# Optimization experiments

Measured on AMD Instinct MI355X. Metric: run time of the kernel, lower is better.

The kernel has to match this reference:

```python
import jax, jax.numpy as jnp
import numpy as np

B, C, H, W = 4, 256, 64, 64
N = H * W


def _conv1x1(x, w, b):
    # x: [B,C,H,W], w: [O,C], b: [O]  (1x1 conv == per-pixel linear)
    return jnp.einsum('bchw,oc->bohw', x, w) + b[None, :, None, None]


def setup_inputs() -> dict:
    key = jax.random.key(0)
    ks = jax.random.split(key, 11)
    s = 1.0 / np.sqrt(C)
    x = jax.random.normal(ks[0], (B, C, H, W), dtype=jnp.float32)
    mkw = lambda k: jax.random.normal(k, (C, C), dtype=jnp.float32) * s
    mkb = lambda k: jax.random.normal(k, (C,), dtype=jnp.float32) * 0.01
    return {
        'x': x,
        'w_teta': mkw(ks[1]), 'b_teta': mkb(ks[2]),
        'w_fi': mkw(ks[3]), 'b_fi': mkb(ks[4]),
        'w_gi': mkw(ks[5]), 'b_gi': mkb(ks[6]),
        'w_o1': mkw(ks[7]), 'b_o1': mkb(ks[8]),
        'w_o2': mkw(ks[9]), 'b_o2': mkb(ks[10]),
    }


def reference(x, w_teta, b_teta, w_fi, b_fi, w_gi, b_gi, w_o1, b_o1, w_o2, b_o2):
    b, c, h, w = x.shape
    n = h * w
    # 1x1 projections, flattened to [B,C,N]
    x1 = _conv1x1(x, w_teta, b_teta).reshape(b, c, n)
    x2 = _conv1x1(x, w_fi, b_fi).reshape(b, c, n)
    x3 = _conv1x1(x, w_gi, b_gi).reshape(b, c, n)
    # NOTE: original uses .view (memory reinterpretation), NOT transpose
    x1 = x1.reshape(b, n, c)
    x3 = x3.reshape(b, n, c)
    scores = jnp.einsum('bnc,bcm->bnm', x1, x2)      # [B,N,N]
    s_row = jax.nn.softmax(scores, axis=2)
    s_col = jax.nn.softmax(scores, axis=1)
    y1 = jnp.einsum('bnm,bmc->bnc', s_row, x3)       # [B,N,C]
    y2 = jnp.einsum('bnm,bmc->bnc', s_col, x3)
    # transpose(1,2) then view -> contiguous transpose + reshape
    y1 = jnp.swapaxes(y1, 1, 2).reshape(b, c, h, w)
    y2 = jnp.swapaxes(y2, 1, 2).reshape(b, c, h, w)
    o1 = _conv1x1(y1, w_o1, b_o1)
    o2 = _conv1x1(y2, w_o2, b_o2)
    xx = jnp.concatenate([x, x], axis=1)             # [B,2C,H,W]
    agg = jnp.concatenate([o1, o2], axis=1)
    return jax.nn.relu(xx + agg)
```

## Files before the change

### kernel.cpp

```cpp
#include <hip/hip_runtime.h>

#define BB   4
#define CC   256
#define NPIX 4096
#define AST2 40
#define YST  72

typedef __attribute__((ext_vector_type(8)))  short bf16x8;
typedef __attribute__((ext_vector_type(8)))  _Float16 f16x8;
typedef __attribute__((ext_vector_type(4)))  short short4v;
typedef __attribute__((ext_vector_type(16))) float f32x16;

__device__ __forceinline__ short f2h(float f) {
    _Float16 h = (_Float16)f;
    return __builtin_bit_cast(short, h);
}
__device__ __forceinline__ int cdrow(int r, int l5) {
    return (r & 3) + 8 * (r >> 2) + 4 * l5;
}
__device__ __forceinline__ short s_enc(float v) {
    float c = fmaxf(fminf(v, 127.9f), -127.9f);
    return (short)__float2int_rn(c * 256.0f);
}
__device__ __forceinline__ float s_dec(short v) {
    return (float)v * (1.0f / 256.0f);
}

__device__ __forceinline__ void mfma_core_f16(
    const short* __restrict__ A, const short* __restrict__ B, f32x16 acc[2][2])
{
    __shared__ short LA[128 * AST2], LB[128 * AST2];
    const int t = threadIdx.x;
    const int lane = t & 63, w = t >> 6;
    const int l31 = lane & 31, l5 = lane >> 5;
    const int nq = (w & 1) * 64, mq = (w >> 1) * 64;
    const int sr = t >> 1;
    const int sk = (t & 1) * 16;
    const size_t gs = (size_t)sr * 256 + sk;
    const int ls = sr * AST2 + sk;

    bf16x8 rA0 = *(const bf16x8*)(A + gs);
    bf16x8 rA1 = *(const bf16x8*)(A + gs + 8);
    bf16x8 rB0 = *(const bf16x8*)(B + gs);
    bf16x8 rB1 = *(const bf16x8*)(B + gs + 8);

    for (int k0 = 0; k0 < 256; k0 += 32) {
        __syncthreads();
        *(bf16x8*)&LA[ls]     = rA0;
        *(bf16x8*)&LA[ls + 8] = rA1;
        *(bf16x8*)&LB[ls]     = rB0;
        *(bf16x8*)&LB[ls + 8] = rB1;
        __syncthreads();
        if (k0 + 32 < 256) {
            size_t g = gs + k0 + 32;
            rA0 = *(const bf16x8*)(A + g);
            rA1 = *(const bf16x8*)(A + g + 8);
            rB0 = *(const bf16x8*)(B + g);
            rB1 = *(const bf16x8*)(B + g + 8);
        }
#pragma unroll
        for (int ks = 0; ks < 2; ks++) {
            f16x8 a[2], b[2];
#pragma unroll
            for (int s = 0; s < 2; s++) {
                a[s] = *(const f16x8*)&LA[(nq + s * 32 + l31) * AST2 + ks * 16 + l5 * 8];
                b[s] = *(const f16x8*)&LB[(mq + s * 32 + l31) * AST2 + ks * 16 + l5 * 8];
            }
#pragma unroll
            for (int s = 0; s < 2; s++)
#pragma unroll
                for (int u = 0; u < 2; u++)
                    acc[s][u] = __builtin_amdgcn_mfma_f32_32x32x16_f16(a[s], b[u], acc[s][u], 0, 0, 0);
        }
    }
}


__global__ __launch_bounds__(256) void pack_w5(
    const float* __restrict__ w0, const float* __restrict__ w1,
    const float* __restrict__ w2, const float* __restrict__ w3,
    const float* __restrict__ w4, short* __restrict__ wall)
{
    int which = blockIdx.y;
    const float* w = which == 0 ? w0 : which == 1 ? w1 : which == 2 ? w2
                   : which == 3 ? w3 : w4;
    int idx = blockIdx.x * 1024 + threadIdx.x * 4;
    float4 v = *(const float4*)(w + idx);
    short4v h;
    h.x = f2h(v.x); h.y = f2h(v.y); h.z = f2h(v.z); h.w = f2h(v.w);
    *(short4v*)(wall + which * 65536 + idx) = h;
}

__global__ __launch_bounds__(256) void pack_t_f16(
    const float* __restrict__ in, short* __restrict__ o16)
{
    __shared__ short T[32][36];
    const int b  = blockIdx.z;
    const int n0 = blockIdx.x * 32;
    const int c0 = blockIdx.y * 32;
    const float* src = in + (size_t)b * CC * NPIX;
    const int t = threadIdx.x;
    const int r = t >> 3, q = t & 7;
    float4 v = *(const float4*)(src + (size_t)(c0 + r) * NPIX + n0 + q * 4);
    T[q * 4 + 0][r] = f2h(v.x);
    T[q * 4 + 1][r] = f2h(v.y);
    T[q * 4 + 2][r] = f2h(v.z);
    T[q * 4 + 3][r] = f2h(v.w);
    __syncthreads();
    short4v o;
    o.x = T[r][q * 4 + 0];
    o.y = T[r][q * 4 + 1];
    o.z = T[r][q * 4 + 2];
    o.w = T[r][q * 4 + 3];
    size_t oo = (size_t)b * CC * NPIX + (size_t)(n0 + r) * 256 + c0 + q * 4;
    *(short4v*)(o16 + oo) = o;
}

__global__ __launch_bounds__(256) void tr16_cn(
    const short* __restrict__ in, short* __restrict__ outp)
{
    __shared__ short T[32][33];
    const int b  = blockIdx.z;
    const int n0 = blockIdx.x * 32;
    const int c0 = blockIdx.y * 32;
    const short* src = in + (size_t)b * CC * NPIX;
    short* dst = outp + (size_t)b * CC * NPIX;
    const int t = threadIdx.x;
    const int r = t >> 3, q = t & 7;
    short4v v = *(const short4v*)(src + (size_t)(c0 + r) * NPIX + n0 + q * 4);
    T[q * 4 + 0][r] = v.x;
    T[q * 4 + 1][r] = v.y;
    T[q * 4 + 2][r] = v.z;
    T[q * 4 + 3][r] = v.w;
    __syncthreads();
    short4v o;
    o.x = T[r][q * 4 + 0];
    o.y = T[r][q * 4 + 1];
    o.z = T[r][q * 4 + 2];
    o.w = T[r][q * 4 + 3];
    *(short4v*)(dst + (size_t)(n0 + r) * 256 + c0 + q * 4) = o;
}

__global__ __launch_bounds__(256) void packVt_bf(
    const short* __restrict__ x3f, short* __restrict__ Vt)
{
    __shared__ short T[32][33];
    const int b  = blockIdx.z;
    const int m0 = blockIdx.x * 32;
    const int c0 = blockIdx.y * 32;
    const short* in = x3f + (size_t)b * CC * NPIX;
    short* out = Vt + (size_t)b * CC * NPIX;
    const int t = threadIdx.x;
    const int r = t >> 3, q = t & 7;
    short4v v = *(const short4v*)(in + (size_t)(m0 + r) * CC + c0 + q * 4);
    T[q * 4 + 0][r] = v.x;
    T[q * 4 + 1][r] = v.y;
    T[q * 4 + 2][r] = v.z;
    T[q * 4 + 3][r] = v.w;
    __syncthreads();
    short4v o;
    o.x = T[r][q * 4 + 0];
    o.y = T[r][q * 4 + 1];
    o.z = T[r][q * 4 + 2];
    o.w = T[r][q * 4 + 3];
    *(short4v*)(out + (size_t)(c0 + r) * NPIX + m0 + q * 4) = o;
}


__global__ __launch_bounds__(256) void proj_mfma(
    const short* __restrict__ wpf, const short* __restrict__ xtf,
    const float* __restrict__ b_teta, const float* __restrict__ b_fi,
    const float* __restrict__ b_gi,
    short* __restrict__ x1f, short* __restrict__ x2f, short* __restrict__ x3f)
{
    const int z = blockIdx.z, p = z >> 2, b = z & 3;
    const int n0 = blockIdx.x * 128, c0 = blockIdx.y * 128;
    const size_t CN = (size_t)CC * NPIX;
    const short* Ah = wpf + p * 65536 + c0 * 256;
    const short* Bh = xtf + (size_t)b * CN + (size_t)n0 * 256;
    const float* bias = p == 0 ? b_teta : p == 1 ? b_fi : b_gi;
    short* dst = p == 0 ? x1f : p == 1 ? x2f : x3f;

    f32x16 acc[2][2] = {};
    mfma_core_f16(Ah, Bh, acc);

    const int t = threadIdx.x, lane = t & 63, w = t >> 6;
    const int l31 = lane & 31, l5 = lane >> 5;
    const int aq = (w & 1) * 64, bq = (w >> 1) * 64;
#pragma unroll
    for (int s = 0; s < 2; s++)
#pragma unroll
        for (int u = 0; u < 2; u++)
#pragma unroll
            for (int r = 0; r < 16; r++) {
                int c = c0 + aq + s * 32 + cdrow(r, l5);
                int n = n0 + bq + u * 32 + l31;
                float v = acc[s][u][r] + bias[c];
                size_t o = (size_t)b * CN + (size_t)c * NPIX + n;
                dst[o] = f2h(v);
            }
}

__global__ __launch_bounds__(256, 2) void scores_mfma(
    const short* __restrict__ x1f, const short* __restrict__ x2tf,
    short* __restrict__ S16, float* __restrict__ pm, float* __restrict__ pl)
{
    __shared__ short LA[256 * AST2];
    __shared__ short LB[128 * AST2];
    const int m0 = blockIdx.x * 128, n0 = blockIdx.y * 256;
    const short* A = x1f + (size_t)n0 * 256;
    const short* B = x2tf + (size_t)m0 * 256;

    const int t = threadIdx.x, lane = t & 63, w = t >> 6;
    const int l31 = lane & 31, l5 = lane >> 5;
    const int h = w & 1, g = w >> 1;

    const size_t gsA = (size_t)t * 256;
    const int lsA = t * AST2;
    const int srB = t >> 1, skB = (t & 1) * 16;
    const size_t gsB = (size_t)srB * 256 + skB;
    const int lsB = srB * AST2 + skB;

    bf16x8 rA0 = *(const bf16x8*)(A + gsA);
    bf16x8 rA1 = *(const bf16x8*)(A + gsA + 8);
    bf16x8 rA2 = *(const bf16x8*)(A + gsA + 16);
    bf16x8 rA3 = *(const bf16x8*)(A + gsA + 24);
    bf16x8 rB0 = *(const bf16x8*)(B + gsB);
    bf16x8 rB1 = *(const bf16x8*)(B + gsB + 8);

    f32x16 acc[4][2] = {};

    for (int k0 = 0; k0 < 256; k0 += 32) {
        __syncthreads();
        *(bf16x8*)&LA[lsA]      = rA0;
        *(bf16x8*)&LA[lsA + 8]  = rA1;
        *(bf16x8*)&LA[lsA + 16] = rA2;
        *(bf16x8*)&LA[lsA + 24] = rA3;
        *(bf16x8*)&LB[lsB]      = rB0;
        *(bf16x8*)&LB[lsB + 8]  = rB1;
        __syncthreads();
        if (k0 + 32 < 256) {
            size_t gA = gsA + k0 + 32;
            size_t gB = gsB + k0 + 32;
            rA0 = *(const bf16x8*)(A + gA);
            rA1 = *(const bf16x8*)(A + gA + 8);
            rA2 = *(const bf16x8*)(A + gA + 16);
            rA3 = *(const bf16x8*)(A + gA + 24);
            rB0 = *(const bf16x8*)(B + gB);
            rB1 = *(const bf16x8*)(B + gB + 8);
        }
#pragma unroll
        for (int ks = 0; ks < 2; ks++) {
            f16x8 a[4], b[2];
#pragma unroll
            for (int s = 0; s < 4; s++)
                a[s] = *(const f16x8*)&LA[(h * 128 + s * 32 + l31) * AST2 + ks * 16 + l5 * 8];
#pragma unroll
            for (int u = 0; u < 2; u++)
                b[u] = *(const f16x8*)&LB[(g * 64 + u * 32 + l31) * AST2 + ks * 16 + l5 * 8];
#pragma unroll
            for (int s = 0; s < 4; s++)
#pragma unroll
                for (int u = 0; u < 2; u++)
                    acc[s][u] = __builtin_amdgcn_mfma_f32_32x32x16_f16(a[s], b[u], acc[s][u], 0, 0, 0);
        }
    }

#pragma unroll
    for (int s = 0; s < 4; s++)
#pragma unroll
        for (int u = 0; u < 2; u++)
#pragma unroll
            for (int r = 0; r < 16; r++) {
                int n = n0 + h * 128 + s * 32 + cdrow(r, l5);
                int m = m0 + g * 64 + u * 32 + l31;
                S16[(size_t)n * NPIX + m] = s_enc(acc[s][u][r]);
            }

#pragma unroll
    for (int u = 0; u < 2; u++) {
        float vmax = -1e30f;
#pragma unroll
        for (int s = 0; s < 4; s++)
#pragma unroll
            for (int r = 0; r < 16; r++) vmax = fmaxf(vmax, acc[s][u][r]);
        float vsum = 0.0f;
#pragma unroll
        for (int s = 0; s < 4; s++)
#pragma unroll
            for (int r = 0; r < 16; r++) vsum += __expf(acc[s][u][r] - vmax);
        float vmax2 = __shfl_xor(vmax, 32, 64);
        float vsum2 = __shfl_xor(vsum, 32, 64);
        float mc = fmaxf(vmax, vmax2);
        float sc = vsum * __expf(vmax - mc) + vsum2 * __expf(vmax2 - mc);
        if (l5 == 0) {
            size_t pidx = (size_t)(blockIdx.y * 2 + h) * NPIX + m0 + g * 64 + u * 32 + l31;
            pm[pidx] = mc;
            pl[pidx] = sc;
        }
    }
}

__global__ __launch_bounds__(256) void out_mfma(
    const short* __restrict__ wof,
    const float* __restrict__ b_o1, const float* __restrict__ b_o2,
    const short* __restrict__ Yp,
    const float* __restrict__ x, float* __restrict__ out, int b)
{
    __shared__ short LA[128 * AST2], LB[128 * AST2];
    const size_t CN_ = (size_t)NPIX * CC;
    const int ch0 = blockIdx.y * 128;
    const int pix0 = blockIdx.x * 128;
    const int mode = ch0 < 256 ? 0 : 1;
    const short* W = wof + mode * 65536 + (size_t)(ch0 & 255) * 256;
    const short* Yq = Yp + (size_t)mode * 8 * CN_;
    const float* bias = mode == 0 ? b_o1 : b_o2;

    const int t = threadIdx.x, lane = t & 63, w = t >> 6;
    const int l31 = lane & 31, l5 = lane >> 5;
    const int nq = (w & 1) * 64, mq = (w >> 1) * 64;
    const int sr = t >> 1;
    const int sk = (t & 1) * 16;
    const size_t gsA = (size_t)sr * 256 + sk;
    const size_t gsB = (size_t)(pix0 + sr) * 256 + sk;
    const int ls = sr * AST2 + sk;

    f32x16 acc[2][2] = {};

    bf16x8 rA0 = *(const bf16x8*)(W + gsA);
    bf16x8 rA1 = *(const bf16x8*)(W + gsA + 8);
    f16x8 rB0, rB1;
    {
        rB0 = *(const f16x8*)(Yq + gsB);
        rB1 = *(const f16x8*)(Yq + gsB + 8);
#pragma unroll
        for (int q = 1; q < 8; q++) {
            rB0 = rB0 + *(const f16x8*)(Yq + (size_t)q * CN_ + gsB);
            rB1 = rB1 + *(const f16x8*)(Yq + (size_t)q * CN_ + gsB + 8);
        }
    }

    for (int k0 = 0; k0 < 256; k0 += 32) {
        __syncthreads();
        *(bf16x8*)&LA[ls]    = rA0;
        *(bf16x8*)&LA[ls + 8] = rA1;
        *(f16x8*)&LB[ls]     = rB0;
        *(f16x8*)&LB[ls + 8] = rB1;
        __syncthreads();
        if (k0 + 32 < 256) {
            size_t gA = gsA + k0 + 32;
            size_t gB = gsB + k0 + 32;
            rA0 = *(const bf16x8*)(W + gA);
            rA1 = *(const bf16x8*)(W + gA + 8);
            rB0 = *(const f16x8*)(Yq + gB);
            rB1 = *(const f16x8*)(Yq + gB + 8);
#pragma unroll
            for (int q = 1; q < 8; q++) {
                rB0 = rB0 + *(const f16x8*)(Yq + (size_t)q * CN_ + gB);
                rB1 = rB1 + *(const f16x8*)(Yq + (size_t)q * CN_ + gB + 8);
            }
        }
#pragma unroll
        for (int ks = 0; ks < 2; ks++) {
            f16x8 a[2], bb[2];
#pragma unroll
            for (int s = 0; s < 2; s++) {
                a[s]  = *(const f16x8*)&LA[(nq + s * 32 + l31) * AST2 + ks * 16 + l5 * 8];
                bb[s] = *(const f16x8*)&LB[(mq + s * 32 + l31) * AST2 + ks * 16 + l5 * 8];
            }
#pragma unroll
            for (int s = 0; s < 2; s++)
#pragma unroll
                for (int u = 0; u < 2; u++)
                    acc[s][u] = __builtin_amdgcn_mfma_f32_32x32x16_f16(a[s], bb[u], acc[s][u], 0, 0, 0);
        }
    }

    const int aq = (w & 1) * 64, bq = (w >> 1) * 64;
#pragma unroll
    for (int s = 0; s < 2; s++)
#pragma unroll
        for (int u = 0; u < 2; u++)
#pragma unroll
            for (int r = 0; r < 16; r++) {
                int ch = ch0 + aq + s * 32 + cdrow(r, l5);
                int pix = pix0 + bq + u * 32 + l31;
                int chm = ch & 255;
                float v = acc[s][u][r] + bias[chm] +
                          x[((size_t)b * CC + chm) * NPIX + pix];
                out[((size_t)b * 2 * CC + ch) * NPIX + pix] = fmaxf(v, 0.0f);
            }
}

__global__ __launch_bounds__(256) void stats16_kernel(
    const short* __restrict__ S16,
    const float* __restrict__ pm, const float* __restrict__ pl,
    float* __restrict__ cm, float* __restrict__ cli,
    float* __restrict__ rm, float* __restrict__ rli)
{
    __shared__ float sm[4][64], sl[4][64];
    __shared__ float red[4];
    const int t = threadIdx.x;
    if (blockIdx.x < 64) {
        const int cl = t & 63, ch = t >> 6;
        const int col = blockIdx.x * 64 + cl;
        float m = -1e30f, l = 0.0f;
        for (int i = ch * 8; i < ch * 8 + 8; i++) {
            float m2 = pm[(size_t)i * NPIX + col];
            float l2 = pl[(size_t)i * NPIX + col];
            float mn = fmaxf(m, m2);
            l = l * __expf(m - mn) + l2 * __expf(m2 - mn);
            m = mn;
        }
        sm[ch][cl] = m;
        sl[ch][cl] = l;
        __syncthreads();
        if (ch == 0) {
#pragma unroll
            for (int j = 1; j < 4; j++) {
                float m2 = sm[j][cl], l2 = sl[j][cl];
                float mn = fmaxf(m, m2);
                l = l * __expf(m - mn) + l2 * __expf(m2 - mn);
                m = mn;
            }
            cm[col]  = m;
            cli[col] = 1.0f / l;
        }
    } else {
        const int row = blockIdx.x - 64;
        const short* sp = S16 + (size_t)row * NPIX;
        const int w = t >> 6, lane = t & 63;
        float s4[16];
#pragma unroll
        for (int i = 0; i < 4; i++) {
            short4v v = *(const short4v*)(sp + (i * 256 + t) * 4);
            s4[i * 4 + 0] = s_dec(v.x);
            s4[i * 4 + 1] = s_dec(v.y);
            s4[i * 4 + 2] = s_dec(v.z);
            s4[i * 4 + 3] = s_dec(v.w);
        }
        float m = -1e30f;
#pragma unroll
        for (int i = 0; i < 16; i++) m = fmaxf(m, s4[i]);
        for (int off = 32; off; off >>= 1) m = fmaxf(m, __shfl_xor(m, off, 64));
        if (lane == 0) red[w] = m;
        __syncthreads();
        m = fmaxf(fmaxf(red[0], red[1]), fmaxf(red[2], red[3]));
        __syncthreads();
        float sum = 0.0f;
#pragma unroll
        for (int i = 0; i < 16; i++) sum += __expf(s4[i] - m);
        for (int off = 32; off; off >>= 1) sum += __shfl_xor(sum, off, 64);
        if (lane == 0) red[w] = sum;
        __syncthreads();
        if (t == 0) {
            rm[row]  = m;
            rli[row] = 1.0f / (red[0] + red[1] + red[2] + red[3]);
        }
    }
}

__global__ __launch_bounds__(256) void pv_kernel(
    const short* __restrict__ S16, const short* __restrict__ Vt,
    const float* __restrict__ rmv, const float* __restrict__ rliv,
    const float* __restrict__ cmv, const float* __restrict__ cliv,
    short* __restrict__ Yp)
{
    __shared__ short LA[128 * YST];
    __shared__ short LB[256 * YST];
    const int mode = blockIdx.z, kq = blockIdx.y;
    const int n0 = blockIdx.x * 128;
    const int kbase = kq * 512;

    const int t = threadIdx.x, lane = t & 63, w = t >> 6;
    const int l31 = lane & 31, l5 = lane >> 5;
    const int nst = (w & 1) * 64, cb = (w >> 1) * 128;
    const int ar = t >> 1;
    const int ak = (t & 1) * 32;
    const int br = t >> 1;
    const int bk = (t & 1) * 32;

    const float mrow = rmv[n0 + ar];
    const float lrow = rliv[n0 + ar];
    const short* sp  = S16 + (size_t)(n0 + ar) * NPIX + kbase + ak;
    const short* vp0 = Vt + (size_t)br * NPIX + kbase + bk;
    const short* vp1 = vp0 + (size_t)128 * NPIX;

    short4v sv[8];
    bf16x8 pb0[2], pb1[2];
#pragma unroll
    for (int i = 0; i < 8; i++)
        sv[i] = *(const short4v*)(sp + i * 4);
#pragma unroll
    for (int j = 0; j < 2; j++) {
        pb0[j] = *(const bf16x8*)(vp0 + j * 16);
        pb1[j] = *(const bf16x8*)(vp1 + j * 16);
    }
    bf16x8 pb0b[2], pb1b[2];
    pb0b[0] = *(const bf16x8*)(vp0 + 8);
    pb0b[1] = *(const bf16x8*)(vp0 + 24);
    pb1b[0] = *(const bf16x8*)(vp1 + 8);
    pb1b[1] = *(const bf16x8*)(vp1 + 24);

    f32x16 acc[2][4] = {};
    for (int s = 0; s < 8; s++) {
        short4v ph[8];
        if (mode == 0) {
#pragma unroll
            for (int i = 0; i < 8; i++) {
                ph[i].x = f2h(__expf(s_dec(sv[i].x) - mrow) * lrow);
                ph[i].y = f2h(__expf(s_dec(sv[i].y) - mrow) * lrow);
                ph[i].z = f2h(__expf(s_dec(sv[i].z) - mrow) * lrow);
                ph[i].w = f2h(__expf(s_dec(sv[i].w) - mrow) * lrow);
            }
        } else {
            const int mg = kbase + s * 64 + ak;
#pragma unroll
            for (int i = 0; i < 8; i++) {
                float4 cm4 = *(const float4*)(cmv + mg + i * 4);
                float4 cl4 = *(const float4*)(cliv + mg + i * 4);
                ph[i].x = f2h(__expf(s_dec(sv[i].x) - cm4.x) * cl4.x);
                ph[i].y = f2h(__expf(s_dec(sv[i].y) - cm4.y) * cl4.y);
                ph[i].z = f2h(__expf(s_dec(sv[i].z) - cm4.z) * cl4.z);
                ph[i].w = f2h(__expf(s_dec(sv[i].w) - cm4.w) * cl4.w);
            }
        }
        __syncthreads();
#pragma unroll
        for (int i = 0; i < 8; i++)
            *(short4v*)&LA[ar * YST + ak + i * 4] = ph[i];
        *(bf16x8*)&LB[br * YST + bk]            = pb0[0];
        *(bf16x8*)&LB[br * YST + bk + 8]        = pb0b[0];
        *(bf16x8*)&LB[br * YST + bk + 16]       = pb0[1];
        *(bf16x8*)&LB[br * YST + bk + 24]       = pb0b[1];
        *(bf16x8*)&LB[(br + 128) * YST + bk]      = pb1[0];
        *(bf16x8*)&LB[(br + 128) * YST + bk + 8]  = pb1b[0];
        *(bf16x8*)&LB[(br + 128) * YST + bk + 16] = pb1[1];
        *(bf16x8*)&LB[(br + 128) * YST + bk + 24] = pb1b[1];
        __syncthreads();
        if (s + 1 < 8) {
            const short* spn = sp + (s + 1) * 64;
#pragma unroll
            for (int i = 0; i < 8; i++)
                sv[i] = *(const short4v*)(spn + i * 4);
            const short* vn0 = vp0 + (s + 1) * 64;
            const short* vn1 = vp1 + (s + 1) * 64;
            pb0[0]  = *(const bf16x8*)(vn0);
            pb0b[0] = *(const bf16x8*)(vn0 + 8);
            pb0[1]  = *(const bf16x8*)(vn0 + 16);
            pb0b[1] = *(const bf16x8*)(vn0 + 24);
            pb1[0]  = *(const bf16x8*)(vn1);
            pb1b[0] = *(const bf16x8*)(vn1 + 8);
            pb1[1]  = *(const bf16x8*)(vn1 + 16);
            pb1b[1] = *(const bf16x8*)(vn1 + 24);
        }
#pragma unroll
        for (int kc = 0; kc < 4; kc++) {
            f16x8 af[2], bf[4];
#pragma unroll
            for (int si = 0; si < 2; si++)
                af[si] = *(const f16x8*)&LA[(nst + si * 32 + l31) * YST + kc * 16 + l5 * 8];
#pragma unroll
            for (int u = 0; u < 4; u++)
                bf[u] = *(const f16x8*)&LB[(cb + u * 32 + l31) * YST + kc * 16 + l5 * 8];
#pragma unroll
            for (int si = 0; si < 2; si++)
#pragma unroll
                for (int u = 0; u < 4; u++)
                    acc[si][u] = __builtin_amdgcn_mfma_f32_32x32x16_f16(af[si], bf[u], acc[si][u], 0, 0, 0);
        }
    }

    short* Yo = Yp + (size_t)(mode * 8 + kq) * ((size_t)NPIX * CC);
#pragma unroll
    for (int si = 0; si < 2; si++)
#pragma unroll
        for (int u = 0; u < 4; u++)
#pragma unroll
            for (int r = 0; r < 16; r++) {
                int rr = cdrow(r, l5);
                Yo[(size_t)(n0 + nst + si * 32 + rr) * CC + cb + u * 32 + l31] = f2h(acc[si][u][r]);
            }
}

extern "C" void kernel_launch(void* const* d_in, const int* in_sizes, int n_in,
                              void* d_out, int out_size, void* d_ws, size_t ws_size,
                              hipStream_t stream)
{
    (void)in_sizes; (void)n_in; (void)out_size; (void)ws_size;
    const float* x      = (const float*)d_in[0];
    const float* w_teta = (const float*)d_in[1];
    const float* b_teta = (const float*)d_in[2];
    const float* w_fi   = (const float*)d_in[3];
    const float* b_fi   = (const float*)d_in[4];
    const float* w_gi   = (const float*)d_in[5];
    const float* b_gi   = (const float*)d_in[6];
    const float* w_o1   = (const float*)d_in[7];
    const float* b_o1   = (const float*)d_in[8];
    const float* w_o2   = (const float*)d_in[9];
    const float* b_o2   = (const float*)d_in[10];
    float* out = (float*)d_out;

    const size_t CN = (size_t)CC * NPIX;
    const size_t NN = (size_t)NPIX * NPIX;
    short* wsp   = (short*)d_ws;
    short* S16   = wsp;
    short* Yp    = S16 + NN;
    short* x1f   = Yp + 16 * CN;
    short* x2tf  = x1f + BB * CN;
    short* Vtb   = x2tf + BB * CN;
    float* cm    = (float*)(Vtb + BB * CN);
    float* cli   = cm + NPIX;
    float* rm    = cli + NPIX;
    float* rli   = rm + NPIX;
    float* pm    = rli + NPIX;
    float* pl    = pm + 64 * NPIX;
    short* wall  = (short*)(pl + 64 * NPIX);
    short* wpf   = wall;
    short* wof   = wall + 3 * 65536;
    short* xtf  = Yp;
    short* x2f  = S16;
    short* x3f  = S16 + BB * CN;

    dim3 blk(256);
    pack_w5<<<dim3(64, 5), blk, 0, stream>>>(w_teta, w_fi, w_gi, w_o1, w_o2, wall);
    pack_t_f16<<<dim3(128, 8, 4), blk, 0, stream>>>(x, xtf);

    proj_mfma<<<dim3(32, 2, 12), blk, 0, stream>>>(
        wpf, xtf, b_teta, b_fi, b_gi, x1f, x2f, x3f);

    tr16_cn<<<dim3(128, 8, 4), blk, 0, stream>>>(x2f, x2tf);
    packVt_bf<<<dim3(128, 8, 4), blk, 0, stream>>>(x3f, Vtb);

    for (int b = 0; b < BB; b++) {
        scores_mfma<<<dim3(32, 16), blk, 0, stream>>>(
            x1f + b * CN, x2tf + b * CN, S16, pm, pl);
        stats16_kernel<<<dim3(64 + NPIX), blk, 0, stream>>>(
            S16, pm, pl, cm, cli, rm, rli);
        pv_kernel<<<dim3(32, 8, 2), blk, 0, stream>>>(
            S16, Vtb + b * CN, rm, rli, cm, cli, Yp);
        out_mfma<<<dim3(32, 4), blk, 0, stream>>>(
            wof, b_o1, b_o2, Yp, x, out, b);
    }
}
```

Before: 475.8 us.

## Rewrite PV kernel to load MFMA operands directly from global, drop LDS staging

The PV kernel no longer stages the probability tile and V tile through shared memory. Each wave computes its own softmax-weighted A fragment in registers and reads B fragments straight from global memory. The tile shape changes to 64 rows by 1024 keys, which halves the K split from 8 to 4 partial outputs, and out_mfma now sums 4 partials instead of 8. This removes LDS writes, barriers and half of the partial-sum traffic. In exchange, V is reread from global by every wave with no shared reuse and nothing is prefetched, so latency hiding now depends on occupancy.

New measurement: 661.5 us. 1.39x slower.

```diff
diff --git a/kernel.cpp b/kernel.cpp
--- a/kernel.cpp
+++ b/kernel.cpp
@@ -313,7 +313,7 @@
     const int pix0 = blockIdx.x * 128;
     const int mode = ch0 < 256 ? 0 : 1;
     const short* W = wof + mode * 65536 + (size_t)(ch0 & 255) * 256;
-    const short* Yq = Yp + (size_t)mode * 8 * CN_;
+    const short* Yq = Yp + (size_t)mode * 4 * CN_;
     const float* bias = mode == 0 ? b_o1 : b_o2;
 
     const int t = threadIdx.x, lane = t & 63, w = t >> 6;
@@ -334,7 +334,7 @@
         rB0 = *(const f16x8*)(Yq + gsB);
         rB1 = *(const f16x8*)(Yq + gsB + 8);
 #pragma unroll
-        for (int q = 1; q < 8; q++) {
+        for (int q = 1; q < 4; q++) {
             rB0 = rB0 + *(const f16x8*)(Yq + (size_t)q * CN_ + gsB);
             rB1 = rB1 + *(const f16x8*)(Yq + (size_t)q * CN_ + gsB + 8);
         }
@@ -355,7 +355,7 @@
             rB0 = *(const f16x8*)(Yq + gB);
             rB1 = *(const f16x8*)(Yq + gB + 8);
 #pragma unroll
-            for (int q = 1; q < 8; q++) {
+            for (int q = 1; q < 4; q++) {
                 rB0 = rB0 + *(const f16x8*)(Yq + (size_t)q * CN_ + gB);
                 rB1 = rB1 + *(const f16x8*)(Yq + (size_t)q * CN_ + gB + 8);
             }
@@ -466,121 +466,72 @@
     const float* __restrict__ cmv, const float* __restrict__ cliv,
     short* __restrict__ Yp)
 {
-    __shared__ short LA[128 * YST];
-    __shared__ short LB[256 * YST];
     const int mode = blockIdx.z, kq = blockIdx.y;
-    const int n0 = blockIdx.x * 128;
-    const int kbase = kq * 512;
+    const int n0 = blockIdx.x * 64;
+    const int kbase = kq * 1024;
 
     const int t = threadIdx.x, lane = t & 63, w = t >> 6;
     const int l31 = lane & 31, l5 = lane >> 5;
-    const int nst = (w & 1) * 64, cb = (w >> 1) * 128;
-    const int ar = t >> 1;
-    const int ak = (t & 1) * 32;
-    const int br = t >> 1;
-    const int bk = (t & 1) * 32;
-
-    const float mrow = rmv[n0 + ar];
-    const float lrow = rliv[n0 + ar];
-    const short* sp  = S16 + (size_t)(n0 + ar) * NPIX + kbase + ak;
-    const short* vp0 = Vt + (size_t)br * NPIX + kbase + bk;
-    const short* vp1 = vp0 + (size_t)128 * NPIX;
-
-    short4v sv[8];
-    bf16x8 pb0[2], pb1[2];
-#pragma unroll
-    for (int i = 0; i < 8; i++)
-        sv[i] = *(const short4v*)(sp + i * 4);
-#pragma unroll
-    for (int j = 0; j < 2; j++) {
-        pb0[j] = *(const bf16x8*)(vp0 + j * 16);
-        pb1[j] = *(const bf16x8*)(vp1 + j * 16);
-    }
-    bf16x8 pb0b[2], pb1b[2];
-    pb0b[0] = *(const bf16x8*)(vp0 + 8);
-    pb0b[1] = *(const bf16x8*)(vp0 + 24);
-    pb1b[0] = *(const bf16x8*)(vp1 + 8);
-    pb1b[1] = *(const bf16x8*)(vp1 + 24);
-
-    f32x16 acc[2][4] = {};
-    for (int s = 0; s < 8; s++) {
-        short4v ph[8];
+    const int nst = (w & 1) * 32, cb = (w >> 1) * 128;
+
+    const int arow = n0 + nst + l31;
+    const float mrow = rmv[arow];
+    const float lrow = rliv[arow];
+    const short* sp = S16 + (size_t)arow * NPIX + kbase + l5 * 8;
+    const short* vb0 = Vt + (size_t)(cb + l31) * NPIX + kbase + l5 * 8;
+    const short* vb1 = vb0 + (size_t)32 * NPIX;
+    const short* vb2 = vb0 + (size_t)64 * NPIX;
+    const short* vb3 = vb0 + (size_t)96 * NPIX;
+    const float* cmp = cmv + kbase + l5 * 8;
+    const float* clp = cliv + kbase + l5 * 8;
+
+    f32x16 acc[4] = {};
+    for (int it = 0; it < 64; it++) {
+        const int kk = it * 16;
+        short4v s0 = *(const short4v*)(sp + kk);
+        short4v s1 = *(const short4v*)(sp + kk + 4);
+        float d[8];
+        d[0] = s_dec(s0.x); d[1] = s_dec(s0.y);
+        d[2] = s_dec(s0.z); d[3] = s_dec(s0.w);
+        d[4] = s_dec(s1.x); d[5] = s_dec(s1.y);
+        d[6] = s_dec(s1.z); d[7] = s_dec(s1.w);
+        f16x8 af;
         if (mode == 0) {
 #pragma unroll
-            for (int i = 0; i < 8; i++) {
-                ph[i].x = f2h(__expf(s_dec(sv[i].x) - mrow) * lrow);
-                ph[i].y = f2h(__expf(s_dec(sv[i].y) - mrow) * lrow);
-                ph[i].z = f2h(__expf(s_dec(sv[i].z) - mrow) * lrow);
-                ph[i].w = f2h(__expf(s_dec(sv[i].w) - mrow) * lrow);
-            }
+            for (int j = 0; j < 8; j++)
+                af[j] = (_Float16)(__expf(d[j] - mrow) * lrow);
         } else {
-            const int mg = kbase + s * 64 + ak;
-#pragma unroll
-            for (int i = 0; i < 8; i++) {
-                float4 cm4 = *(const float4*)(cmv + mg + i * 4);
-                float4 cl4 = *(const float4*)(cliv + mg + i * 4);
-                ph[i].x = f2h(__expf(s_dec(sv[i].x) - cm4.x) * cl4.x);
-                ph[i].y = f2h(__expf(s_dec(sv[i].y) - cm4.y) * cl4.y);
-                ph[i].z = f2h(__expf(s_dec(sv[i].z) - cm4.z) * cl4.z);
-                ph[i].w = f2h(__expf(s_dec(sv[i].w) - cm4.w) * cl4.w);
-            }
-        }
-        __syncthreads();
-#pragma unroll
-        for (int i = 0; i < 8; i++)
-            *(short4v*)&LA[ar * YST + ak + i * 4] = ph[i];
-        *(bf16x8*)&LB[br * YST + bk]            = pb0[0];
-        *(bf16x8*)&LB[br * YST + bk + 8]        = pb0b[0];
-        *(bf16x8*)&LB[br * YST + bk + 16]       = pb0[1];
-        *(bf16x8*)&LB[br * YST + bk + 24]       = pb0b[1];
-        *(bf16x8*)&LB[(br + 128) * YST + bk]      = pb1[0];
-        *(bf16x8*)&LB[(br + 128) * YST + bk + 8]  = pb1b[0];
-        *(bf16x8*)&LB[(br + 128) * YST + bk + 16] = pb1[1];
-        *(bf16x8*)&LB[(br + 128) * YST + bk + 24] = pb1b[1];
-        __syncthreads();
-        if (s + 1 < 8) {
-            const short* spn = sp + (s + 1) * 64;
-#pragma unroll
-            for (int i = 0; i < 8; i++)
-                sv[i] = *(const short4v*)(spn + i * 4);
-            const short* vn0 = vp0 + (s + 1) * 64;
-            const short* vn1 = vp1 + (s + 1) * 64;
-            pb0[0]  = *(const bf16x8*)(vn0);
-            pb0b[0] = *(const bf16x8*)(vn0 + 8);
-            pb0[1]  = *(const bf16x8*)(vn0 + 16);
-            pb0b[1] = *(const bf16x8*)(vn0 + 24);
-            pb1[0]  = *(const bf16x8*)(vn1);
-            pb1b[0] = *(const bf16x8*)(vn1 + 8);
-            pb1[1]  = *(const bf16x8*)(vn1 + 16);
-            pb1b[1] = *(const bf16x8*)(vn1 + 24);
-        }
-#pragma unroll
-        for (int kc = 0; kc < 4; kc++) {
-            f16x8 af[2], bf[4];
-#pragma unroll
-            for (int si = 0; si < 2; si++)
-                af[si] = *(const f16x8*)&LA[(nst + si * 32 + l31) * YST + kc * 16 + l5 * 8];
-#pragma unroll
-            for (int u = 0; u < 4; u++)
-                bf[u] = *(const f16x8*)&LB[(cb + u * 32 + l31) * YST + kc * 16 + l5 * 8];
-#pragma unroll
-            for (int si = 0; si < 2; si++)
-#pragma unroll
-                for (int u = 0; u < 4; u++)
-                    acc[si][u] = __builtin_amdgcn_mfma_f32_32x32x16_f16(af[si], bf[u], acc[si][u], 0, 0, 0);
-        }
-    }
-
-    short* Yo = Yp + (size_t)(mode * 8 + kq) * ((size_t)NPIX * CC);
-#pragma unroll
-    for (int si = 0; si < 2; si++)
-#pragma unroll
-        for (int u = 0; u < 4; u++)
-#pragma unroll
-            for (int r = 0; r < 16; r++) {
-                int rr = cdrow(r, l5);
-                Yo[(size_t)(n0 + nst + si * 32 + rr) * CC + cb + u * 32 + l31] = f2h(acc[si][u][r]);
-            }
+            float4 cm0 = *(const float4*)(cmp + kk);
+            float4 cm1 = *(const float4*)(cmp + kk + 4);
+            float4 cl0 = *(const float4*)(clp + kk);
+            float4 cl1 = *(const float4*)(clp + kk + 4);
+            af[0] = (_Float16)(__expf(d[0] - cm0.x) * cl0.x);
+            af[1] = (_Float16)(__expf(d[1] - cm0.y) * cl0.y);
+            af[2] = (_Float16)(__expf(d[2] - cm0.z) * cl0.z);
+            af[3] = (_Float16)(__expf(d[3] - cm0.w) * cl0.w);
+            af[4] = (_Float16)(__expf(d[4] - cm1.x) * cl1.x);
+            af[5] = (_Float16)(__expf(d[5] - cm1.y) * cl1.y);
+            af[6] = (_Float16)(__expf(d[6] - cm1.z) * cl1.z);
+            af[7] = (_Float16)(__expf(d[7] - cm1.w) * cl1.w);
+        }
+        f16x8 bf0 = *(const f16x8*)(vb0 + kk);
+        f16x8 bf1 = *(const f16x8*)(vb1 + kk);
+        f16x8 bf2 = *(const f16x8*)(vb2 + kk);
+        f16x8 bf3 = *(const f16x8*)(vb3 + kk);
+        acc[0] = __builtin_amdgcn_mfma_f32_32x32x16_f16(af, bf0, acc[0], 0, 0, 0);
+        acc[1] = __builtin_amdgcn_mfma_f32_32x32x16_f16(af, bf1, acc[1], 0, 0, 0);
+        acc[2] = __builtin_amdgcn_mfma_f32_32x32x16_f16(af, bf2, acc[2], 0, 0, 0);
+        acc[3] = __builtin_amdgcn_mfma_f32_32x32x16_f16(af, bf3, acc[3], 0, 0, 0);
+    }
+
+    short* Yo = Yp + (size_t)(mode * 4 + kq) * ((size_t)NPIX * CC);
+#pragma unroll
+    for (int u = 0; u < 4; u++)
+#pragma unroll
+        for (int r = 0; r < 16; r++) {
+            int rr = cdrow(r, l5);
+            Yo[(size_t)(n0 + nst + rr) * CC + cb + u * 32 + l31] = f2h(acc[u][r]);
+        }
 }
 
 extern "C" void kernel_launch(void* const* d_in, const int* in_sizes, int n_in,
@@ -637,7 +588,7 @@
             x1f + b * CN, x2tf + b * CN, S16, pm, pl);
         stats16_kernel<<<dim3(64 + NPIX), blk, 0, stream>>>(
             S16, pm, pl, cm, cli, rm, rli);
-        pv_kernel<<<dim3(32, 8, 2), blk, 0, stream>>>(
+        pv_kernel<<<dim3(64, 4, 2), blk, 0, stream>>>(
             S16, Vtb + b * CN, rm, rli, cm, cli, Yp);
         out_mfma<<<dim3(32, 4), blk, 0, stream>>>(
             wof, b_o1, b_o2, Yp, x, out, b);
```
